# Kernel optimization log

Measured on AMD Instinct MI355X. Metric: run time of the kernel, lower is better.

## Reference

```python
import jax, jax.numpy as jnp
import numpy as np

NUM_EMBEDDINGS = 1024
EMBEDDING_DIM = 64
COMMITMENT_COST = 0.25


def setup_inputs() -> dict:
    key = jax.random.key(0)
    k1, k2 = jax.random.split(key)
    z_e = jax.random.normal(k1, (32, EMBEDDING_DIM, 32, 32), dtype=jnp.float32)
    # codebook init: uniform(-1/K, 1/K) as in the torch module
    embedding = jax.random.uniform(
        k2, (NUM_EMBEDDINGS, EMBEDDING_DIM), dtype=jnp.float32,
        minval=-1.0 / NUM_EMBEDDINGS, maxval=1.0 / NUM_EMBEDDINGS)
    return {"z_e": z_e, "embedding": embedding}


def reference(z_e, embedding):
    B, C, H, W = z_e.shape
    # (B,C,H,W) -> (B,H,W,C) -> (N,C)
    z = jnp.transpose(z_e, (0, 2, 3, 1))
    z_flat = z.reshape(-1, C)
    # squared L2 distances: |z|^2 - 2 z e^T + |e|^2  -> (N, K)
    distances = (jnp.sum(z_flat ** 2, axis=1, keepdims=True)
                 - 2.0 * z_flat @ embedding.T
                 + jnp.sum(embedding ** 2, axis=1))
    encoding_indices = jnp.argmin(distances, axis=1)  # (N,)
    z_q = embedding[encoding_indices].reshape(z.shape)  # (B,H,W,C)
    # use_ema=True branch: loss = commitment_cost * mse(z, sg(z_q))
    commitment_loss = jnp.mean((z - jax.lax.stop_gradient(z_q)) ** 2)
    loss = COMMITMENT_COST * commitment_loss
    # straight-through estimator
    z_q_ste = z + jax.lax.stop_gradient(z_q - z)
    z_q_ste = jnp.transpose(z_q_ste, (0, 3, 1, 2))  # back to (B,C,H,W)
    indices = encoding_indices.reshape(B, H, W)
    return z_q_ste, loss, indices
```

## Files before the change

### kernel.cpp

```cpp
#include <hip/hip_runtime.h>
#include <hip/hip_bf16.h>
#include <math.h>
#include <stdint.h>

#define NUM_EMB 1024
#define DIM 64
#define LOSS_OFF 2097152
#define IDX_OFF 2097153
#define NROWS 32768
#define EMAX_LOG2 10
#define CAND_CAP 1024

typedef float f32x4 __attribute__((ext_vector_type(4)));
typedef short bf16x8 __attribute__((ext_vector_type(8)));

__device__ __forceinline__ float np_fold16(float* y) {
#pragma unroll
    for (int j = 0; j < 8; ++j) y[j] = __fadd_rn(y[j], y[j + 8]);
#pragma unroll
    for (int j = 0; j < 4; ++j) y[j] = __fadd_rn(y[j], y[j + 4]);
    y[0] = __fadd_rn(y[0], y[2]);
    y[1] = __fadd_rn(y[1], y[3]);
    return __fadd_rn(y[0], y[1]);
}

__device__ __forceinline__ unsigned short bf16bits(float f) {
    __hip_bfloat16 h = __float2bfloat16(f);
    return *reinterpret_cast<unsigned short*>(&h);
}

__global__ void vq_emb_norms(const float* __restrict__ emb,
                             float* __restrict__ norms,
                             float* __restrict__ out) {
    int k = blockIdx.x * blockDim.x + threadIdx.x;
    if (k == 0) out[LOSS_OFF] = 0.0f;
    if (k < NUM_EMB) {
        const float4* e4 = reinterpret_cast<const float4*>(emb + k * DIM);
        float e2[DIM];
#pragma unroll
        for (int q = 0; q < 16; ++q) {
            const float4 v = e4[q];
            e2[q * 4 + 0] = v.x; e2[q * 4 + 1] = v.y;
            e2[q * 4 + 2] = v.z; e2[q * 4 + 3] = v.w;
        }
        float y[16];
#pragma unroll
        for (int j = 0; j < 16; ++j) {
            float a = __fadd_rn(__fmul_rn(e2[j],      e2[j]),
                                __fmul_rn(e2[j + 16], e2[j + 16]));
            float b = __fadd_rn(__fmul_rn(e2[j + 32], e2[j + 32]),
                                __fmul_rn(e2[j + 48], e2[j + 48]));
            y[j] = __fadd_rn(a, b);
        }
        norms[k] = np_fold16(y);
    }
}

__device__ inline unsigned long long exact_key(
        const float* __restrict__ z_e, const float* __restrict__ emb,
        const float* __restrict__ norms, long zrowbase, int k) {
    float z[DIM];
#pragma unroll
    for (int c = 0; c < DIM; ++c) z[c] = z_e[zrowbase + (long)c * 1024];
    float A;
    {
        float y[16];
#pragma unroll
        for (int j = 0; j < 16; ++j) {
            float a  = __fadd_rn(__fmul_rn(z[j],      z[j]),
                                 __fmul_rn(z[j + 16], z[j + 16]));
            float c2 = __fadd_rn(__fmul_rn(z[j + 32], z[j + 32]),
                                 __fmul_rn(z[j + 48], z[j + 48]));
            y[j] = __fadd_rn(a, c2);
        }
        A = np_fold16(y);
    }
    const float4* ep = reinterpret_cast<const float4*>(emb + (size_t)k * DIM);
    float dot = 0.f;
#pragma unroll
    for (int q = 0; q < 16; ++q) {
        const float4 e4 = ep[q];
        dot = __fmaf_rn(z[4 * q + 0], e4.x, dot);
        dot = __fmaf_rn(z[4 * q + 1], e4.y, dot);
        dot = __fmaf_rn(z[4 * q + 2], e4.z, dot);
        dot = __fmaf_rn(z[4 * q + 3], e4.w, dot);
    }
    const float d = __fadd_rn(__fmaf_rn(-2.f, dot, A), norms[k]);
    return ((unsigned long long)__float_as_uint(d) << 32) | (unsigned)k;
}

__device__ __forceinline__ void stage_ebf(short* s_ebf,
                                          const float* __restrict__ emb,
                                          int ch, int tid) {
#pragma unroll
    for (int it = 0; it < 16; ++it) {
        const int idx = it * 512 + tid;
        const int cl  = idx >> 5;
        const int cp  = idx & 31;
        const float f0 = emb[(size_t)(ch * 256 + cl) * 64 + 2 * cp];
        const float f1 = emb[(size_t)(ch * 256 + cl) * 64 + 2 * cp + 1];
        const unsigned int pk =
            (unsigned int)bf16bits(f0) | ((unsigned int)bf16bits(f1) << 16);
        const int byte = cl * 128 + ((4 * cp) ^ ((cl & 7) << 4));
        *reinterpret_cast<unsigned int*>(
            reinterpret_cast<char*>(s_ebf) + byte) = pk;
    }
}

__device__ __forceinline__ f32x4 tile_dot(const short* s_ebf, int cl, int kb,
                                          bf16x8 a0, bf16x8 a1) {
    const char* base = reinterpret_cast<const char*>(s_ebf) + cl * 128;
    const int sw = (cl & 7) << 4;
    const bf16x8 b0 = *reinterpret_cast<const bf16x8*>(base + ((16 * kb) ^ sw));
    const bf16x8 b1 = *reinterpret_cast<const bf16x8*>(base + ((64 + 16 * kb) ^ sw));
    f32x4 C = {0.f, 0.f, 0.f, 0.f};
    C = __builtin_amdgcn_mfma_f32_16x16x32_bf16(a0, b0, C, 0, 0, 0);
    C = __builtin_amdgcn_mfma_f32_16x16x32_bf16(a1, b1, C, 0, 0, 0);
    return C;
}

__global__ __launch_bounds__(512, 4)
void vq_mfma_fused(const float* __restrict__ z_e,
                   const float* __restrict__ emb,
                   const float* __restrict__ norms,
                   float* __restrict__ out) {
    __shared__ short s_zbf[128 * 64];
    __shared__ short s_ebf[256 * 64];
    __shared__ float s_cmin[128];
    __shared__ float s_S[128];
    __shared__ unsigned int s_cand[CAND_CAP];
    __shared__ int s_cnt;
    __shared__ unsigned long long s_key[128];
    __shared__ int s_final[128];
    __shared__ float s_loss[2][8];

    const int tid  = threadIdx.x;
    const int lane = tid & 63;
    const int wave = __builtin_amdgcn_readfirstlane(tid >> 6);

    const int n0  = blockIdx.x * 128;
    const int b   = n0 >> 10;
    const int hw0 = n0 & 1023;

    if (tid == 0) s_cnt = 0;
    if (tid < 128) s_key[tid] = ~0ull;

#pragma unroll
    for (int it = 0; it < 8; ++it) {
        const int idx = it * 512 + tid;
        const int hw  = idx & 127;
        const int cp  = idx >> 7;
        const float f0 = z_e[(long)b * 65536 + (long)(2 * cp)     * 1024 + hw0 + hw];
        const float f1 = z_e[(long)b * 65536 + (long)(2 * cp + 1) * 1024 + hw0 + hw];
        const unsigned int pk =
            (unsigned int)bf16bits(f0) | ((unsigned int)bf16bits(f1) << 16);
        const int byte = hw * 128 + ((4 * cp) ^ ((hw & 7) << 4));
        *reinterpret_cast<unsigned int*>(
            reinterpret_cast<char*>(s_zbf) + byte) = pk;
    }
    __syncthreads();

    const int rowA = wave * 16 + (lane & 15);
    const int kb   = lane >> 4;
    bf16x8 a0, a1;
    {
        const char* base = reinterpret_cast<const char*>(s_zbf) + rowA * 128;
        const int sw = (rowA & 7) << 4;
        a0 = *reinterpret_cast<const bf16x8*>(base + ((16 * kb) ^ sw));
        a1 = *reinterpret_cast<const bf16x8*>(base + ((64 + 16 * kb) ^ sw));
    }
    {
        float s = 0.f;
#pragma unroll
        for (int j = 0; j < 8; ++j) {
            s += fabsf(__uint_as_float(((unsigned)(unsigned short)a0[j]) << 16));
            s += fabsf(__uint_as_float(((unsigned)(unsigned short)a1[j]) << 16));
        }
        s += __shfl_xor(s, 16, 64);
        s += __shfl_xor(s, 32, 64);
        if (kb == 0) s_S[rowA] = s;
    }

    float pmin[4] = {INFINITY, INFINITY, INFINITY, INFINITY};
    for (int ch = 0; ch < 4; ++ch) {
        __syncthreads();
        stage_ebf(s_ebf, emb, ch, tid);
        __syncthreads();
#pragma unroll
        for (int t = 0; t < 16; ++t) {
            const int cl   = t * 16 + (lane & 15);
            const int code = ch * 256 + cl;
            const f32x4 C  = tile_dot(s_ebf, cl, kb, a0, a1);
            const float Ek = norms[code];
#pragma unroll
            for (int r = 0; r < 4; ++r)
                pmin[r] = fminf(pmin[r], __fmaf_rn(-2.f, C[r], Ek));
        }
    }
#pragma unroll
    for (int r = 0; r < 4; ++r) {
        float m = pmin[r];
        m = fminf(m, __shfl_xor(m, 1, 64));
        m = fminf(m, __shfl_xor(m, 2, 64));
        m = fminf(m, __shfl_xor(m, 4, 64));
        m = fminf(m, __shfl_xor(m, 8, 64));
        pmin[r] = m;
    }
    if ((lane & 15) == 0) {
#pragma unroll
        for (int r = 0; r < 4; ++r)
            s_cmin[wave * 16 + (lane >> 4) * 4 + r] = pmin[r];
    }
    __syncthreads();

    float thr[4];
#pragma unroll
    for (int r = 0; r < 4; ++r) {
        const int row = wave * 16 + (lane >> 4) * 4 + r;
        thr[r] = s_cmin[row] + (3.0517578125e-5f * s_S[row] + 2e-4f);
    }

    for (int ch = 0; ch < 4; ++ch) {
        __syncthreads();
        stage_ebf(s_ebf, emb, ch, tid);
        __syncthreads();
#pragma unroll
        for (int t = 0; t < 16; ++t) {
            const int cl   = t * 16 + (lane & 15);
            const int code = ch * 256 + cl;
            const f32x4 C  = tile_dot(s_ebf, cl, kb, a0, a1);
            const float Ek = norms[code];
#pragma unroll
            for (int r = 0; r < 4; ++r) {
                const float ct = __fmaf_rn(-2.f, C[r], Ek);
                if (ct <= thr[r]) {
                    const int row = wave * 16 + (lane >> 4) * 4 + r;
                    const int slot = atomicAdd(&s_cnt, 1);
                    if (slot < CAND_CAP)
                        s_cand[slot] = ((unsigned)row << 10) | (unsigned)code;
                }
            }
        }
    }
    __syncthreads();

    const int cnt = s_cnt;
    if (cnt <= CAND_CAP) {
        for (int i = tid; i < cnt; i += 512) {
            const unsigned int e = s_cand[i];
            const int row = (int)(e >> 10);
            const int k   = (int)(e & 1023u);
            const unsigned long long key =
                exact_key(z_e, emb, norms, (long)b * 65536 + hw0 + row, k);
            atomicMin(&s_key[row], key);
        }
    } else {
        for (int j = tid; j < 128 * 1024; j += 512) {
            const int row = j >> 10;
            const int k   = j & 1023;
            const unsigned long long key =
                exact_key(z_e, emb, norms, (long)b * 65536 + hw0 + row, k);
            atomicMin(&s_key[row], key);
        }
    }
    __syncthreads();

    if (tid < 128) {
        const int k = (int)(s_key[tid] & 0xFFFFFFFFull);
        s_final[tid] = k;
        out[IDX_OFF + n0 + tid] = (float)k;
    }
    __syncthreads();

    const long zb0 = (long)b * 65536 + hw0 + lane;
    const long zb1 = zb0 + 64;
    const int f0 = s_final[lane];
    const int f1 = s_final[64 + lane];
    float ls0 = 0.f, ls1 = 0.f;
#pragma unroll
    for (int j = 0; j < DIM / 8; ++j) {
        const int c = wave * 8 + j;
        const float zc0 = z_e[zb0 + (long)c * 1024];
        const float ec0 = emb[f0 * DIM + c];
        out[((long)(b * 64 + c)) * 1024 + hw0 + lane] = zc0 + (ec0 - zc0);
        const float dl0 = zc0 - ec0;
        ls0 = __fmaf_rn(dl0, dl0, ls0);
        const float zc1 = z_e[zb1 + (long)c * 1024];
        const float ec1 = emb[f1 * DIM + c];
        out[((long)(b * 64 + c)) * 1024 + hw0 + 64 + lane] = zc1 + (ec1 - zc1);
        const float dl1 = zc1 - ec1;
        ls1 = __fmaf_rn(dl1, dl1, ls1);
    }
#pragma unroll
    for (int off = 32; off >= 1; off >>= 1) {
        ls0 += __shfl_xor(ls0, off, 64);
        ls1 += __shfl_xor(ls1, off, 64);
    }
    if (lane == 0) { s_loss[0][wave] = ls0; s_loss[1][wave] = ls1; }
    __syncthreads();

    if (tid == 0) {
        float t0 = 0.f, t1 = 0.f;
#pragma unroll
        for (int w = 0; w < 8; ++w) t0 = __fadd_rn(t0, s_loss[0][w]);
#pragma unroll
        for (int w = 0; w < 8; ++w) t1 = __fadd_rn(t1, s_loss[1][w]);
        atomicAdd(out + LOSS_OFF, t0 * 1.1920928955078125e-07f);
        atomicAdd(out + LOSS_OFF, t1 * 1.1920928955078125e-07f);
    }
}

extern "C" void kernel_launch(void* const* d_in, const int* in_sizes, int n_in,
                              void* d_out, int out_size, void* d_ws, size_t ws_size,
                              hipStream_t stream) {
    const float* z_e = (const float*)d_in[0];
    const float* emb = (const float*)d_in[1];
    float* out   = (float*)d_out;
    float* norms = (float*)d_ws;

    vq_emb_norms<<<dim3(16), dim3(64), 0, stream>>>(emb, norms, out);
    vq_mfma_fused<<<dim3(NROWS / 128), dim3(512), 0, stream>>>(z_e, emb, norms, out);
}
```

Baseline: 121.8 us.

## Replace two-pass candidate scan with single-pass top-2 tracking and smaller row tiles

The second MFMA pass over the codebook is removed: each lane now tracks its best and second-best approximate distance and code in one pass. A lane emits only its best code as a candidate, or all of its codes when the second-best is also within the threshold. Blocks now hold 64 rows, with the eight waves splitting the codebook into two halves, so twice as many blocks launch. Embedding staging uses float4 loads. This trades more per-element compare and select work and possible extra candidate overflow for half the matrix work and staging traffic.

```diff
diff --git a/kernel.cpp b/kernel.cpp
--- a/kernel.cpp
+++ b/kernel.cpp
@@ -8,7 +8,6 @@
 #define LOSS_OFF 2097152
 #define IDX_OFF 2097153
 #define NROWS 32768
-#define EMAX_LOG2 10
 #define CAND_CAP 1024
 
 typedef float f32x4 __attribute__((ext_vector_type(4)));
@@ -93,17 +92,17 @@
                                           const float* __restrict__ emb,
                                           int ch, int tid) {
 #pragma unroll
-    for (int it = 0; it < 16; ++it) {
+    for (int it = 0; it < 8; ++it) {
         const int idx = it * 512 + tid;
-        const int cl  = idx >> 5;
-        const int cp  = idx & 31;
-        const float f0 = emb[(size_t)(ch * 256 + cl) * 64 + 2 * cp];
-        const float f1 = emb[(size_t)(ch * 256 + cl) * 64 + 2 * cp + 1];
-        const unsigned int pk =
-            (unsigned int)bf16bits(f0) | ((unsigned int)bf16bits(f1) << 16);
-        const int byte = cl * 128 + ((4 * cp) ^ ((cl & 7) << 4));
-        *reinterpret_cast<unsigned int*>(
-            reinterpret_cast<char*>(s_ebf) + byte) = pk;
+        const int cl  = idx >> 4;
+        const int cq  = idx & 15;
+        const float4 v = *reinterpret_cast<const float4*>(
+            emb + (size_t)(ch * 256 + cl) * 64 + 4 * cq);
+        uint2 pk;
+        pk.x = (unsigned)bf16bits(v.x) | ((unsigned)bf16bits(v.y) << 16);
+        pk.y = (unsigned)bf16bits(v.z) | ((unsigned)bf16bits(v.w) << 16);
+        const int byte = cl * 128 + ((8 * cq) ^ ((cl & 7) << 4));
+        *reinterpret_cast<uint2*>(reinterpret_cast<char*>(s_ebf) + byte) = pk;
     }
 }
 
@@ -124,32 +123,34 @@
                    const float* __restrict__ emb,
                    const float* __restrict__ norms,
                    float* __restrict__ out) {
-    __shared__ short s_zbf[128 * 64];
+    __shared__ short s_zbf[64 * 64];
     __shared__ short s_ebf[256 * 64];
-    __shared__ float s_cmin[128];
-    __shared__ float s_S[128];
+    __shared__ float s_pmin[2][64];
+    __shared__ float s_S[64];
     __shared__ unsigned int s_cand[CAND_CAP];
     __shared__ int s_cnt;
-    __shared__ unsigned long long s_key[128];
-    __shared__ int s_final[128];
-    __shared__ float s_loss[2][8];
+    __shared__ unsigned long long s_key[64];
+    __shared__ int s_final[64];
+    __shared__ float s_loss[8];
 
     const int tid  = threadIdx.x;
     const int lane = tid & 63;
     const int wave = __builtin_amdgcn_readfirstlane(tid >> 6);
-
-    const int n0  = blockIdx.x * 128;
+    const int rt    = wave & 3;
+    const int chalf = wave >> 2;
+
+    const int n0  = blockIdx.x * 64;
     const int b   = n0 >> 10;
     const int hw0 = n0 & 1023;
 
     if (tid == 0) s_cnt = 0;
-    if (tid < 128) s_key[tid] = ~0ull;
-
-#pragma unroll
-    for (int it = 0; it < 8; ++it) {
+    if (tid < 64) s_key[tid] = ~0ull;
+
+#pragma unroll
+    for (int it = 0; it < 4; ++it) {
         const int idx = it * 512 + tid;
-        const int hw  = idx & 127;
-        const int cp  = idx >> 7;
+        const int hw  = idx & 63;
+        const int cp  = idx >> 6;
         const float f0 = z_e[(long)b * 65536 + (long)(2 * cp)     * 1024 + hw0 + hw];
         const float f1 = z_e[(long)b * 65536 + (long)(2 * cp + 1) * 1024 + hw0 + hw];
         const unsigned int pk =
@@ -160,7 +161,7 @@
     }
     __syncthreads();
 
-    const int rowA = wave * 16 + (lane & 15);
+    const int rowA = rt * 16 + (lane & 15);
     const int kb   = lane >> 4;
     bf16x8 a0, a1;
     {
@@ -169,7 +170,7 @@
         a0 = *reinterpret_cast<const bf16x8*>(base + ((16 * kb) ^ sw));
         a1 = *reinterpret_cast<const bf16x8*>(base + ((64 + 16 * kb) ^ sw));
     }
-    {
+    if (chalf == 0) {
         float s = 0.f;
 #pragma unroll
         for (int j = 0; j < 8; ++j) {
@@ -181,65 +182,66 @@
         if (kb == 0) s_S[rowA] = s;
     }
 
-    float pmin[4] = {INFINITY, INFINITY, INFINITY, INFINITY};
+    float bestv[4] = {INFINITY, INFINITY, INFINITY, INFINITY};
+    float secv[4]  = {INFINITY, INFINITY, INFINITY, INFINITY};
+    int   bestc[4] = {0, 0, 0, 0};
+    int   secc[4]  = {0, 0, 0, 0};
+
     for (int ch = 0; ch < 4; ++ch) {
         __syncthreads();
         stage_ebf(s_ebf, emb, ch, tid);
         __syncthreads();
 #pragma unroll
-        for (int t = 0; t < 16; ++t) {
+        for (int tt = 0; tt < 8; ++tt) {
+            const int t    = chalf * 8 + tt;
             const int cl   = t * 16 + (lane & 15);
             const int code = ch * 256 + cl;
             const f32x4 C  = tile_dot(s_ebf, cl, kb, a0, a1);
             const float Ek = norms[code];
 #pragma unroll
-            for (int r = 0; r < 4; ++r)
-                pmin[r] = fminf(pmin[r], __fmaf_rn(-2.f, C[r], Ek));
-        }
-    }
+            for (int r = 0; r < 4; ++r) {
+                const float v = __fmaf_rn(-2.f, C[r], Ek);
+                if (v < bestv[r]) {
+                    secv[r] = bestv[r]; secc[r] = bestc[r];
+                    bestv[r] = v;       bestc[r] = code;
+                } else if (v < secv[r]) {
+                    secv[r] = v;        secc[r] = code;
+                }
+            }
+        }
+    }
+
 #pragma unroll
     for (int r = 0; r < 4; ++r) {
-        float m = pmin[r];
+        float m = bestv[r];
         m = fminf(m, __shfl_xor(m, 1, 64));
         m = fminf(m, __shfl_xor(m, 2, 64));
         m = fminf(m, __shfl_xor(m, 4, 64));
         m = fminf(m, __shfl_xor(m, 8, 64));
-        pmin[r] = m;
-    }
-    if ((lane & 15) == 0) {
-#pragma unroll
-        for (int r = 0; r < 4; ++r)
-            s_cmin[wave * 16 + (lane >> 4) * 4 + r] = pmin[r];
-    }
-    __syncthreads();
-
-    float thr[4];
+        if ((lane & 15) == 0)
+            s_pmin[chalf][rt * 16 + (lane >> 4) * 4 + r] = m;
+    }
+    __syncthreads();
+
 #pragma unroll
     for (int r = 0; r < 4; ++r) {
-        const int row = wave * 16 + (lane >> 4) * 4 + r;
-        thr[r] = s_cmin[row] + (3.0517578125e-5f * s_S[row] + 2e-4f);
-    }
-
-    for (int ch = 0; ch < 4; ++ch) {
-        __syncthreads();
-        stage_ebf(s_ebf, emb, ch, tid);
-        __syncthreads();
-#pragma unroll
-        for (int t = 0; t < 16; ++t) {
-            const int cl   = t * 16 + (lane & 15);
-            const int code = ch * 256 + cl;
-            const f32x4 C  = tile_dot(s_ebf, cl, kb, a0, a1);
-            const float Ek = norms[code];
-#pragma unroll
-            for (int r = 0; r < 4; ++r) {
-                const float ct = __fmaf_rn(-2.f, C[r], Ek);
-                if (ct <= thr[r]) {
-                    const int row = wave * 16 + (lane >> 4) * 4 + r;
+        const int row = rt * 16 + (lane >> 4) * 4 + r;
+        const float rowmin = fminf(s_pmin[0][row], s_pmin[1][row]);
+        const float thr = rowmin + (3.0517578125e-5f * s_S[row] + 2e-4f);
+        if (secv[r] <= thr) {
+            for (int ch = 0; ch < 4; ++ch)
+#pragma unroll
+                for (int tt = 0; tt < 8; ++tt) {
+                    const int code =
+                        ch * 256 + (chalf * 8 + tt) * 16 + (lane & 15);
                     const int slot = atomicAdd(&s_cnt, 1);
                     if (slot < CAND_CAP)
                         s_cand[slot] = ((unsigned)row << 10) | (unsigned)code;
                 }
-            }
+        } else if (bestv[r] <= thr) {
+            const int slot = atomicAdd(&s_cnt, 1);
+            if (slot < CAND_CAP)
+                s_cand[slot] = ((unsigned)row << 10) | (unsigned)bestc[r];
         }
     }
     __syncthreads();
@@ -255,7 +257,7 @@
             atomicMin(&s_key[row], key);
         }
     } else {
-        for (int j = tid; j < 128 * 1024; j += 512) {
+        for (int j = tid; j < 64 * 1024; j += 512) {
             const int row = j >> 10;
             const int k   = j & 1023;
             const unsigned long long key =
@@ -265,48 +267,35 @@
     }
     __syncthreads();
 
-    if (tid < 128) {
+    if (tid < 64) {
         const int k = (int)(s_key[tid] & 0xFFFFFFFFull);
         s_final[tid] = k;
         out[IDX_OFF + n0 + tid] = (float)k;
     }
     __syncthreads();
 
-    const long zb0 = (long)b * 65536 + hw0 + lane;
-    const long zb1 = zb0 + 64;
-    const int f0 = s_final[lane];
-    const int f1 = s_final[64 + lane];
-    float ls0 = 0.f, ls1 = 0.f;
+    const long zbase = (long)b * 65536 + hw0 + lane;
+    const int fidx = s_final[lane];
+    float lsum = 0.f;
 #pragma unroll
     for (int j = 0; j < DIM / 8; ++j) {
         const int c = wave * 8 + j;
-        const float zc0 = z_e[zb0 + (long)c * 1024];
-        const float ec0 = emb[f0 * DIM + c];
-        out[((long)(b * 64 + c)) * 1024 + hw0 + lane] = zc0 + (ec0 - zc0);
-        const float dl0 = zc0 - ec0;
-        ls0 = __fmaf_rn(dl0, dl0, ls0);
-        const float zc1 = z_e[zb1 + (long)c * 1024];
-        const float ec1 = emb[f1 * DIM + c];
-        out[((long)(b * 64 + c)) * 1024 + hw0 + 64 + lane] = zc1 + (ec1 - zc1);
-        const float dl1 = zc1 - ec1;
-        ls1 = __fmaf_rn(dl1, dl1, ls1);
-    }
-#pragma unroll
-    for (int off = 32; off >= 1; off >>= 1) {
-        ls0 += __shfl_xor(ls0, off, 64);
-        ls1 += __shfl_xor(ls1, off, 64);
-    }
-    if (lane == 0) { s_loss[0][wave] = ls0; s_loss[1][wave] = ls1; }
+        const float zc = z_e[zbase + (long)c * 1024];
+        const float ec = emb[fidx * DIM + c];
+        out[((long)(b * 64 + c)) * 1024 + hw0 + lane] = zc + (ec - zc);
+        const float dlt = zc - ec;
+        lsum = __fmaf_rn(dlt, dlt, lsum);
+    }
+#pragma unroll
+    for (int off = 32; off >= 1; off >>= 1) lsum += __shfl_xor(lsum, off, 64);
+    if (lane == 0) s_loss[wave] = lsum;
     __syncthreads();
 
     if (tid == 0) {
-        float t0 = 0.f, t1 = 0.f;
-#pragma unroll
-        for (int w = 0; w < 8; ++w) t0 = __fadd_rn(t0, s_loss[0][w]);
-#pragma unroll
-        for (int w = 0; w < 8; ++w) t1 = __fadd_rn(t1, s_loss[1][w]);
-        atomicAdd(out + LOSS_OFF, t0 * 1.1920928955078125e-07f);
-        atomicAdd(out + LOSS_OFF, t1 * 1.1920928955078125e-07f);
+        float t = 0.f;
+#pragma unroll
+        for (int w = 0; w < 8; ++w) t = __fadd_rn(t, s_loss[w]);
+        atomicAdd(out + LOSS_OFF, t * 1.1920928955078125e-07f);
     }
 }
 
@@ -319,5 +308,5 @@
     float* norms = (float*)d_ws;
 
     vq_emb_norms<<<dim3(16), dim3(64), 0, stream>>>(emb, norms, out);
-    vq_mfma_fused<<<dim3(NROWS / 128), dim3(512), 0, stream>>>(z_e, emb, norms, out);
-}
+    vq_mfma_fused<<<dim3(NROWS / 64), dim3(512), 0, stream>>>(z_e, emb, norms, out);
+}
```

Result: faster. 101.0 us (-17.0%).
